# Performance work log

Hardware: AMD Instinct MI355X
Metric: run time of the kernel (lower is better)

The kernel has to match this reference:

```python
import jax, jax.numpy as jnp
import numpy as np

N = 50000
E = 800000
IN_DIM = 128
HID = 128
HEADS = 8
OUT_DIM = 64
NEG_SLOPE = 0.2


def setup_inputs() -> dict:
    key = jax.random.key(0)
    ks = jax.random.split(key, 10)
    x = jax.random.normal(ks[0], (N, IN_DIM), dtype=jnp.float32)
    edge_index = jax.random.randint(ks[1], (2, E), 0, N, dtype=jnp.int64)
    c1 = HID // HEADS  # 16 per-head channels, layer 1
    # layer 1 params (GATConv: lin has no bias; att_src/att_dst are [1,H,C])
    W1 = jax.random.normal(ks[2], (IN_DIM, HEADS * c1), dtype=jnp.float32) * 0.1
    att_src1 = jax.random.normal(ks[3], (1, HEADS, c1), dtype=jnp.float32) * 0.1
    att_dst1 = jax.random.normal(ks[4], (1, HEADS, c1), dtype=jnp.float32) * 0.1
    b1 = jnp.zeros((HEADS * c1,), dtype=jnp.float32)  # concat=True -> bias size H*C
    # layer 2 params (heads=1, concat=False)
    W2 = jax.random.normal(ks[5], (HID, OUT_DIM), dtype=jnp.float32) * 0.1
    att_src2 = jax.random.normal(ks[6], (1, 1, OUT_DIM), dtype=jnp.float32) * 0.1
    att_dst2 = jax.random.normal(ks[7], (1, 1, OUT_DIM), dtype=jnp.float32) * 0.1
    b2 = jnp.zeros((OUT_DIM,), dtype=jnp.float32)
    return {"x": x, "edge_index": edge_index,
            "W1": W1, "att_src1": att_src1, "att_dst1": att_dst1, "b1": b1,
            "W2": W2, "att_src2": att_src2, "att_dst2": att_dst2, "b2": b2}


def _gat_conv(x, src, dst, W, att_src, att_dst, bias, heads, concat):
    n = x.shape[0]
    c = W.shape[1] // heads
    h = (x @ W).reshape(n, heads, c)                      # [N,H,C]
    a_src = jnp.sum(h * att_src, axis=-1)                 # [N,H]
    a_dst = jnp.sum(h * att_dst, axis=-1)                 # [N,H]
    e = a_src[src] + a_dst[dst]                           # [E,H]
    e = jnp.where(e > 0, e, NEG_SLOPE * e)                # leaky_relu
    # segment softmax over incoming edges of each dst node
    m = jax.ops.segment_max(e, dst, num_segments=n)       # [N,H]
    ex = jnp.exp(e - m[dst])
    denom = jax.ops.segment_sum(ex, dst, num_segments=n)  # [N,H]
    alpha = ex / (denom[dst] + 1e-16)                     # [E,H]
    msg = h[src] * alpha[:, :, None]                      # [E,H,C]
    out = jax.ops.segment_sum(msg, dst, num_segments=n)   # [N,H,C]
    out = out.reshape(n, heads * c) if concat else out.mean(axis=1)
    return out + bias


def reference(x, edge_index, W1, att_src1, att_dst1, b1, W2, att_src2, att_dst2, b2):
    # add self-loops (PyG GATConv default add_self_loops=True)
    loops = jnp.arange(N, dtype=edge_index.dtype)
    src = jnp.concatenate([edge_index[0], loops])
    dst = jnp.concatenate([edge_index[1], loops])
    h = _gat_conv(x, src, dst, W1, att_src1, att_dst1, b1, HEADS, True)
    h = jax.nn.elu(h)
    out = _gat_conv(h, src, dst, W2, att_src2, att_dst2, b2, 1, False)
    return jax.nn.log_softmax(out, axis=1)
```

## Files before the change

### kernel.cpp

```cpp
#include <hip/hip_runtime.h>
#include <math.h>

#define N_NODES 50000
#define E_EDGES 800000
#define ET      (E_EDGES + N_NODES)
#define IN_DIM  128
#define HID     128
#define HEADS   8
#define C1      16
#define OUT_DIM 64
#define NEG_SLOPE 0.2f
#define LOG2E   1.4426950408889634f

#define TILE    8192
#define NT      ((ET + TILE - 1) / TILE)
#define NB      ((N_NODES + 255) / 256)

#define CONV_BLOCKS (N_NODES * IN_DIM / 4 / 256)
#define PREP_BLOCKS 112
#define MEGA_A (NT + CONV_BLOCKS + PREP_BLOCKS)
#define L1T_BLOCKS ((N_NODES + 63) / 64)
#define MEGA_B (NB + L1T_BLOCKS)
#define FUSE_BLOCKS ((N_NODES + 15) / 16)

typedef unsigned int uint32;
typedef __attribute__((ext_vector_type(8))) short bf16x8;
typedef __attribute__((ext_vector_type(4))) float f32x4;
typedef __attribute__((ext_vector_type(2))) float f32x2;

static __device__ __forceinline__ unsigned short f2bf(float f) {
    uint32 u = __float_as_uint(f);
    u += 0x7FFFu + ((u >> 16) & 1u);
    return (unsigned short)(u >> 16);
}

static __device__ __forceinline__ unsigned char f2fp8(float f) {
    int pk = __builtin_amdgcn_cvt_pk_fp8_f32(f, f, 0, false);
    return (unsigned char)(pk & 0xFF);
}


__global__ __launch_bounds__(256) void prep_all(
        const int* __restrict__ dst, int* __restrict__ cnt,
        const float* __restrict__ x, unsigned short* __restrict__ xb,
        const float* __restrict__ W1, const float* __restrict__ as1,
        const float* __restrict__ ad1, const float* __restrict__ W2,
        const float* __restrict__ as2, const float* __restrict__ ad2,
        unsigned short* __restrict__ w1t, unsigned short* __restrict__ p1t,
        unsigned short* __restrict__ w2t, unsigned short* __restrict__ p2t) {
    __shared__ int hist[NB];
    int blk = blockIdx.x, t = threadIdx.x;
    if (blk < NT) {
        for (int b = t; b < NB; b += 256) hist[b] = 0;
        __syncthreads();
        int base = blk * TILE;
        #pragma unroll
        for (int it = 0; it < TILE / 256; ++it) {
            int i = base + it * 256 + t;
            if (i < ET) {
                int d = (i < E_EDGES) ? dst[i] : (i - E_EDGES);
                atomicAdd(&hist[d >> 8], 1);
            }
        }
        __syncthreads();
        for (int b = t; b < NB; b += 256) cnt[blk * NB + b] = hist[b];
    } else if (blk < NT + CONV_BLOCKS) {
        int i = (blk - NT) * 256 + t;
        float4 v = ((const float4*)x)[i];
        ushort4 o;
        o.x = f2bf(v.x); o.y = f2bf(v.y); o.z = f2bf(v.z); o.w = f2bf(v.w);
        ((ushort4*)xb)[i] = o;
    } else {
        int b = blk - NT - CONV_BLOCKS;
        if (b < 64) {
            int i = b * 256 + t;
            int n = i >> 7, k = i & 127;
            w1t[n * IN_DIM + k] = f2bf(W1[k * HID + n]);
        } else if (b < 96) {
            int i = (b - 64) * 256 + t;
            int n = i >> 7, k = i & 127;
            w2t[n * HID + k] = f2bf(W2[k * OUT_DIM + n]);
        } else if (b < 104) {
            int i = (b - 96) * 256 + t;
            int j = i >> 7, k = i & 127;
            int hh = j & 7;
            const float* a = (j < 8) ? as1 : ad1;
            float acc = 0.f;
            #pragma unroll
            for (int c = 0; c < C1; ++c)
                acc = fmaf(W1[k * HID + hh * C1 + c], a[hh * C1 + c], acc);
            p1t[j * IN_DIM + k] = f2bf(acc * LOG2E);
        } else {
            int i = (b - 104) * 256 + t;
            int j = i >> 7, k = i & 127;
            if (j < 2) {
                const float* a = (j == 0) ? as2 : ad2;
                float acc = 0.f;
                #pragma unroll
                for (int c = 0; c < OUT_DIM; ++c)
                    acc = fmaf(W2[k * OUT_DIM + c], a[c], acc);
                p2t[j * HID + k] = f2bf(acc * LOG2E);
            } else {
                p2t[j * HID + k] = 0;
            }
        }
    }
}


__global__ __launch_bounds__(256) void bucket_scatter(
        const int* __restrict__ src, const int* __restrict__ dst,
        const int* __restrict__ cnt, int* __restrict__ bucketStart,
        uint32* __restrict__ pairs) {
    __shared__ int lcur[NB];
    __shared__ int sscan[256];
    int t = threadIdx.x;
    int tile = blockIdx.x;

    int run = 0, total = 0;
    if (t < NB) {
        for (int k = 0; k < NT; ++k) {
            int c = cnt[k * NB + t];
            if (k < tile) run += c;
            total += c;
        }
    }
    sscan[t] = (t < NB) ? total : 0;
    __syncthreads();
    #pragma unroll
    for (int off = 1; off < 256; off <<= 1) {
        int add = (t >= off) ? sscan[t - off] : 0;
        __syncthreads();
        sscan[t] += add;
        __syncthreads();
    }
    int bstart = sscan[t] - total;
    if (t < NB) {
        lcur[t] = bstart + run;
        if (tile == 0) bucketStart[t] = bstart;
    }
    if (tile == 0 && t == 0) bucketStart[NB] = ET;
    __syncthreads();

    int base = tile * TILE;
    #pragma unroll
    for (int it = 0; it < TILE / 256; ++it) {
        int i = base + it * 256 + t;
        if (i < ET) {
            int s, d;
            if (i < E_EDGES) { s = src[i]; d = dst[i]; }
            else             { s = d = i - E_EDGES; }
            int pos = atomicAdd(&lcur[d >> 8], 1);
            pairs[pos] = ((uint32)s << 8) | (uint32)(d & 255);
        }
    }
}


__global__ __launch_bounds__(256) void build_l1t(
        const uint32* __restrict__ pairs, const int* __restrict__ bucketStart,
        int* __restrict__ row_start, int* __restrict__ csr_src,
        const unsigned short* __restrict__ xb, const unsigned short* __restrict__ w1t,
        const unsigned short* __restrict__ p1t, unsigned char* __restrict__ h1f,
        float* __restrict__ a_src, float* __restrict__ a_dst) {
    __shared__ int sdeg[256];
    __shared__ int sscan[256];
    int t = threadIdx.x;
    if (blockIdx.x < NB) {
        int b = blockIdx.x;
        int beg = bucketStart[b], end = bucketStart[b + 1];
        sdeg[t] = 0;
        __syncthreads();
        for (int j = beg + t; j < end; j += 256)
            atomicAdd(&sdeg[pairs[j] & 255u], 1);
        __syncthreads();
        int v = sdeg[t];
        sscan[t] = v;
        __syncthreads();
        #pragma unroll
        for (int off = 1; off < 256; off <<= 1) {
            int add = (t >= off) ? sscan[t - off] : 0;
            __syncthreads();
            sscan[t] += add;
            __syncthreads();
        }
        int pos0 = beg + sscan[t] - v;
        int n = b * 256 + t;
        if (n < N_NODES) row_start[n] = pos0;
        if (b == 0 && t == 0) row_start[N_NODES] = ET;
        __syncthreads();
        sscan[t] = pos0;
        __syncthreads();
        for (int j = beg + t; j < end; j += 256) {
            uint32 p = pairs[j];
            int pos = atomicAdd(&sscan[p & 255u], 1);
            csr_src[pos] = (int)(p >> 8);
        }
        return;
    }
    int bb = blockIdx.x - NB;
    int w = t >> 6, lane = t & 63;
    int l15 = lane & 15, quad = lane >> 4;
    int n0 = bb * 64 + w * 16;
    int mrow = n0 + l15;
    int mload = (mrow < N_NODES) ? mrow : (N_NODES - 1);

    bf16x8 af[4];
    #pragma unroll
    for (int s = 0; s < 4; ++s)
        af[s] = *(const bf16x8*)&xb[(size_t)mload * IN_DIM + s * 32 + quad * 8];

    #pragma unroll
    for (int tt = 0; tt < 9; ++tt) {
        const unsigned short* Brow = (tt < 8) ? &w1t[(tt * 16 + l15) * IN_DIM]
                                              : &p1t[l15 * IN_DIM];
        f32x4 acc = {0.f, 0.f, 0.f, 0.f};
        #pragma unroll
        for (int s = 0; s < 4; ++s) {
            bf16x8 bf = *(const bf16x8*)&Brow[s * 32 + quad * 8];
            acc = __builtin_amdgcn_mfma_f32_16x16x32_bf16(af[s], bf, acc, 0, 0, 0);
        }
        int nodeb = n0 + quad * 4;
        if (tt < 8) {
            int ch = tt * 16 + l15;
            #pragma unroll
            for (int r = 0; r < 4; ++r)
                if (nodeb + r < N_NODES)
                    h1f[(size_t)(nodeb + r) * HID + ch] = f2fp8(acc[r]);
        } else {
            #pragma unroll
            for (int r = 0; r < 4; ++r) {
                if (nodeb + r < N_NODES) {
                    if (l15 < 8) a_src[(nodeb + r) * HEADS + l15] = acc[r];
                    else         a_dst[(nodeb + r) * HEADS + (l15 - 8)] = acc[r];
                }
            }
        }
    }
}


__global__ __launch_bounds__(256) void l1agg_l2t(
        const unsigned char* __restrict__ h1f, const float* __restrict__ a_src,
        const float* __restrict__ a_dst, const int* __restrict__ row_start,
        const int* __restrict__ csr_src, const float* __restrict__ b1,
        const unsigned short* __restrict__ w2t, const unsigned short* __restrict__ p2t,
        unsigned char* __restrict__ h2f, float* __restrict__ a_src2,
        float* __restrict__ a_dst2) {
    __shared__ unsigned short ha[16][128];
    __shared__ int sdeg16[16];
    __shared__ unsigned char perm[16];
    int t = threadIdx.x;
    int w = t >> 6;
    uint32 lane = t & 63;
    uint32 quarter = lane >> 4;
    uint32 lane16 = lane & 15;
    int n0blk = blockIdx.x * 16;

    if (t < 16) {
        int n = n0blk + t;
        int nc = (n < N_NODES) ? n : (N_NODES - 1);
        sdeg16[t] = row_start[nc + 1] - row_start[nc];
    }
    __syncthreads();
    if (t < 16) {
        int d = sdeg16[t];
        int r = 0;
        #pragma unroll
        for (int j = 0; j < 16; ++j) {
            int dj = sdeg16[j];
            r += (dj < d) || (dj == d && j < t);
        }
        perm[r] = (unsigned char)t;
    }
    __syncthreads();

    {
        uint32 c0 = lane16 * 8u;
        uint32 h = lane16 >> 1;
        int n_local = (int)perm[w * 4 + (int)quarter];
        int n = n0blk + n_local;
        int nc = (n < N_NODES) ? n : (N_NODES - 1);
        int beg = row_start[nc], end = row_start[nc + 1];
        int cnt = end - beg;
        int kmax = cnt;
        kmax = max(kmax, __shfl_xor(kmax, 16, 64));
        kmax = max(kmax, __shfl_xor(kmax, 32, 64));
        float adst = a_dst[nc * HEADS + h];
        float l = 0.f;
        float a0 = 0.f, a1 = 0.f, a2 = 0.f, a3 = 0.f;
        float a4 = 0.f, a5 = 0.f, a6 = 0.f, a7 = 0.f;

        auto edge = [&](float e0, uint2 u0, bool live) {
            float e = e0 + adst;
            e = fmaxf(e, NEG_SLOPE * e);
            e = live ? e : -10000.f;
            float p = exp2f(e);
            l += p;
            f32x2 f01 = __builtin_amdgcn_cvt_pk_f32_fp8((int)u0.x, false);
            f32x2 f23 = __builtin_amdgcn_cvt_pk_f32_fp8((int)u0.x, true);
            f32x2 f45 = __builtin_amdgcn_cvt_pk_f32_fp8((int)u0.y, false);
            f32x2 f67 = __builtin_amdgcn_cvt_pk_f32_fp8((int)u0.y, true);
            a0 = fmaf(p, f01[0], a0);
            a1 = fmaf(p, f01[1], a1);
            a2 = fmaf(p, f23[0], a2);
            a3 = fmaf(p, f23[1], a3);
            a4 = fmaf(p, f45[0], a4);
            a5 = fmaf(p, f45[1], a5);
            a6 = fmaf(p, f67[0], a6);
            a7 = fmaf(p, f67[1], a7);
        };

        int k = 0;
        for (; k + 8 <= kmax; k += 8) {
            uint32 ss[8]; float ee[8]; uint2 uu[8];
            #pragma unroll
            for (int q = 0; q < 8; ++q) {
                int j = beg + k + q;
                int jc = (j < end) ? j : (end - 1);
                ss[q] = (uint32)csr_src[jc];
            }
            #pragma unroll
            for (int q = 0; q < 8; ++q) ee[q] = a_src[ss[q] * 8u + h];
            #pragma unroll
            for (int q = 0; q < 8; ++q) uu[q] = *(const uint2*)&h1f[(ss[q] << 7) + c0];
            #pragma unroll
            for (int q = 0; q < 8; ++q) edge(ee[q], uu[q], k + q < cnt);
        }
        for (; k < kmax; k += 4) {
            uint32 ss[4]; float ee[4]; uint2 uu[4];
            #pragma unroll
            for (int q = 0; q < 4; ++q) {
                int j = beg + k + q;
                int jc = (j < end) ? j : (end - 1);
                ss[q] = (uint32)csr_src[jc];
            }
            #pragma unroll
            for (int q = 0; q < 4; ++q) ee[q] = a_src[ss[q] * 8u + h];
            #pragma unroll
            for (int q = 0; q < 4; ++q) uu[q] = *(const uint2*)&h1f[(ss[q] << 7) + c0];
            #pragma unroll
            for (int q = 0; q < 4; ++q) edge(ee[q], uu[q], k + q < cnt);
        }

        float inv = 1.f / (l + 1e-16f);
        float v0 = a0 * inv + b1[c0 + 0];
        float v1 = a1 * inv + b1[c0 + 1];
        float v2 = a2 * inv + b1[c0 + 2];
        float v3 = a3 * inv + b1[c0 + 3];
        float v4 = a4 * inv + b1[c0 + 4];
        float v5 = a5 * inv + b1[c0 + 5];
        float v6 = a6 * inv + b1[c0 + 6];
        float v7 = a7 * inv + b1[c0 + 7];
        v0 = v0 > 0.f ? v0 : (__expf(v0) - 1.f);
        v1 = v1 > 0.f ? v1 : (__expf(v1) - 1.f);
        v2 = v2 > 0.f ? v2 : (__expf(v2) - 1.f);
        v3 = v3 > 0.f ? v3 : (__expf(v3) - 1.f);
        v4 = v4 > 0.f ? v4 : (__expf(v4) - 1.f);
        v5 = v5 > 0.f ? v5 : (__expf(v5) - 1.f);
        v6 = v6 > 0.f ? v6 : (__expf(v6) - 1.f);
        v7 = v7 > 0.f ? v7 : (__expf(v7) - 1.f);
        uint4 packed;
        packed.x = (uint32)f2bf(v0) | ((uint32)f2bf(v1) << 16);
        packed.y = (uint32)f2bf(v2) | ((uint32)f2bf(v3) << 16);
        packed.z = (uint32)f2bf(v4) | ((uint32)f2bf(v5) << 16);
        packed.w = (uint32)f2bf(v6) | ((uint32)f2bf(v7) << 16);
        uint32 g = lane16 ^ ((uint32)n_local & 15u);
        *(uint4*)&ha[n_local][g * 8] = packed;
    }
    __syncthreads();

    {
        int l15 = (int)lane16, quad = (int)quarter;
        int n0 = n0blk;
        int nloc = l15;

        bf16x8 af[4];
        #pragma unroll
        for (int s = 0; s < 4; ++s) {
            uint32 g = (uint32)(s * 4 + quad) ^ (uint32)l15;
            af[s] = *(const bf16x8*)&ha[nloc][g * 8];
        }

        #pragma unroll
        for (int pass = 0; pass < 2; ++pass) {
            if (pass == 1 && w != 0) break;
            int tt = (pass == 0) ? w : 4;
            const unsigned short* Brow = (tt < 4) ? &w2t[(tt * 16 + l15) * HID]
                                                  : &p2t[l15 * HID];
            f32x4 acc = {0.f, 0.f, 0.f, 0.f};
            #pragma unroll
            for (int s = 0; s < 4; ++s) {
                bf16x8 bf = *(const bf16x8*)&Brow[s * 32 + quad * 8];
                acc = __builtin_amdgcn_mfma_f32_16x16x32_bf16(af[s], bf, acc, 0, 0, 0);
            }
            int nodeb = n0 + quad * 4;
            if (tt < 4) {
                int ch = tt * 16 + l15;
                #pragma unroll
                for (int r = 0; r < 4; ++r)
                    if (nodeb + r < N_NODES)
                        h2f[(size_t)(nodeb + r) * OUT_DIM + ch] = f2fp8(acc[r]);
            } else {
                #pragma unroll
                for (int r = 0; r < 4; ++r) {
                    if (nodeb + r < N_NODES) {
                        if (l15 == 0) a_src2[nodeb + r] = acc[r];
                        else if (l15 == 1) a_dst2[nodeb + r] = acc[r];
                    }
                }
            }
        }
    }
}


__global__ __launch_bounds__(128) void l2_aggregate(
        const unsigned char* __restrict__ h2f, const float* __restrict__ a_src2,
        const float* __restrict__ a_dst2, const int* __restrict__ row_start,
        const int* __restrict__ csr_src, const float* __restrict__ b2,
        float* __restrict__ out) {
    __shared__ int sdeg8[8];
    __shared__ int perm8[8];
    int t = threadIdx.x;
    int w = t >> 6;
    uint32 lane = t & 63;
    uint32 quarter = lane >> 4;
    uint32 lane16 = lane & 15;
    int nbase = blockIdx.x * 8;
    if (t < 8)
        sdeg8[t] = row_start[nbase + t + 1] - row_start[nbase + t];
    __syncthreads();
    if (t < 8) {
        int d = sdeg8[t];
        int r = 0;
        #pragma unroll
        for (int j = 0; j < 8; ++j) {
            int dj = sdeg8[j];
            r += (dj < d) || (dj == d && j < t);
        }
        perm8[r] = t;
    }
    __syncthreads();
    int n = nbase + perm8[w * 4 + (int)quarter];
    uint32 c0 = lane16 * 4u;
    int beg = row_start[n], end = row_start[n + 1];
    int cnt = end - beg;
    int kmax = cnt;
    kmax = max(kmax, __shfl_xor(kmax, 16, 64));
    kmax = max(kmax, __shfl_xor(kmax, 32, 64));
    float adst = a_dst2[n];
    float l = 0.f, a0 = 0.f, a1 = 0.f, a2 = 0.f, a3 = 0.f;

    for (int k = 0; k < kmax; k += 4) {
        uint32 ss[4]; float ee[4]; uint32 uu[4];
        #pragma unroll
        for (int q = 0; q < 4; ++q) {
            int j = beg + k + q;
            int jc = (j < end) ? j : (end - 1);
            ss[q] = (uint32)csr_src[jc];
        }
        #pragma unroll
        for (int q = 0; q < 4; ++q) ee[q] = a_src2[ss[q]];
        #pragma unroll
        for (int q = 0; q < 4; ++q) uu[q] = *(const uint32*)&h2f[(ss[q] << 6) + c0];
        #pragma unroll
        for (int q = 0; q < 4; ++q) {
            float e = ee[q] + adst;
            e = fmaxf(e, NEG_SLOPE * e);
            e = (k + q < cnt) ? e : -10000.f;
            float p = exp2f(e);
            l += p;
            f32x2 f01 = __builtin_amdgcn_cvt_pk_f32_fp8((int)uu[q], false);
            f32x2 f23 = __builtin_amdgcn_cvt_pk_f32_fp8((int)uu[q], true);
            a0 = fmaf(p, f01[0], a0);
            a1 = fmaf(p, f01[1], a1);
            a2 = fmaf(p, f23[0], a2);
            a3 = fmaf(p, f23[1], a3);
        }
    }

    float inv = 1.f / (l + 1e-16f);
    float o0 = a0 * inv + b2[c0 + 0];
    float o1 = a1 * inv + b2[c0 + 1];
    float o2 = a2 * inv + b2[c0 + 2];
    float o3 = a3 * inv + b2[c0 + 3];
    float mx = fmaxf(fmaxf(o0, o1), fmaxf(o2, o3));
    #pragma unroll
    for (int m = 8; m > 0; m >>= 1) mx = fmaxf(mx, __shfl_xor(mx, m, 16));
    float ex = __expf(o0 - mx) + __expf(o1 - mx) + __expf(o2 - mx) + __expf(o3 - mx);
    #pragma unroll
    for (int m = 8; m > 0; m >>= 1) ex += __shfl_xor(ex, m, 16);
    float lse = mx + __logf(ex);
    float4 o = make_float4(o0 - lse, o1 - lse, o2 - lse, o3 - lse);
    *(float4*)&out[(size_t)n * OUT_DIM + c0] = o;
}


extern "C" void kernel_launch(void* const* d_in, const int* in_sizes, int n_in,
                              void* d_out, int out_size, void* d_ws, size_t ws_size,
                              hipStream_t stream) {
    const float* x   = (const float*)d_in[0];
    const int*   ei  = (const int*)d_in[1];
    const float* W1  = (const float*)d_in[2];
    const float* as1 = (const float*)d_in[3];
    const float* ad1 = (const float*)d_in[4];
    const float* b1  = (const float*)d_in[5];
    const float* W2  = (const float*)d_in[6];
    const float* as2 = (const float*)d_in[7];
    const float* ad2 = (const float*)d_in[8];
    const float* b2  = (const float*)d_in[9];
    float* out = (float*)d_out;

    const int* src = ei;
    const int* dst = ei + E_EDGES;

    char* ws = (char*)d_ws;
    size_t off = 0;
    auto alloc = [&](size_t bytes) -> void* {
        void* p = ws + off;
        off += (bytes + 255) & ~size_t(255);
        return p;
    };
    unsigned short* xb     = (unsigned short*)alloc((size_t)N_NODES * IN_DIM * 2);
    unsigned char*  h1f    = (unsigned char*)alloc((size_t)N_NODES * HID);
    unsigned char*  h2f    = (unsigned char*)alloc((size_t)N_NODES * OUT_DIM);
    unsigned short* w1t    = (unsigned short*)alloc((size_t)HID * IN_DIM * 2);
    unsigned short* p1t    = (unsigned short*)alloc((size_t)16 * IN_DIM * 2);
    unsigned short* w2t    = (unsigned short*)alloc((size_t)OUT_DIM * HID * 2);
    unsigned short* p2t    = (unsigned short*)alloc((size_t)16 * HID * 2);
    float* a_src1    = (float*)alloc((size_t)N_NODES * HEADS * 4);
    float* a_dst1    = (float*)alloc((size_t)N_NODES * HEADS * 4);
    float* a_src2    = (float*)alloc((size_t)N_NODES * 4);
    float* a_dst2    = (float*)alloc((size_t)N_NODES * 4);
    int*   row_start = (int*)alloc((size_t)(N_NODES + 1) * 4);
    int*   csr_src   = (int*)alloc((size_t)ET * 4);
    uint32* pairs    = (uint32*)alloc((size_t)ET * 4);
    int*   cnt       = (int*)alloc((size_t)NB * NT * 4);
    int*   bucketStart = (int*)alloc((size_t)(NB + 1) * 4);

    prep_all<<<MEGA_A, 256, 0, stream>>>(dst, cnt, x, xb, W1, as1, ad1,
                                         W2, as2, ad2, w1t, p1t, w2t, p2t);
    bucket_scatter<<<NT, 256, 0, stream>>>(src, dst, cnt, bucketStart, pairs);
    build_l1t<<<MEGA_B, 256, 0, stream>>>(pairs, bucketStart, row_start, csr_src,
                                          xb, w1t, p1t, h1f, a_src1, a_dst1);
    l1agg_l2t<<<FUSE_BLOCKS, 256, 0, stream>>>(h1f, a_src1, a_dst1, row_start, csr_src,
                                               b1, w2t, p2t, h2f, a_src2, a_dst2);
    l2_aggregate<<<N_NODES / 8, 128, 0, stream>>>(h2f, a_src2, a_dst2, row_start, csr_src, b2, out);
}
```

Before: 191.9 us.

## Split layer-1 transform across scatter and bucket kernels; prefetch CSR indices

Moves the layer-1 MFMA transform into a shared device function and splits its blocks between the bucket-scatter kernel (391 blocks) and the CSR build kernel (the rest). This balances work across the two launches so the transform overlaps the lightweight scatter phase. Both aggregation kernels now prefetch the next batch of 8 CSR source indices while the current batch is processed. The layer-2 aggregation also moves to 256-thread blocks of 16 nodes with an 8-edge unrolled loop. The changes add register pressure, and the gains depend on scheduling across kernels.

Result: faster. 187.8 us (-2.1%).

```diff
diff --git a/kernel.cpp b/kernel.cpp
--- a/kernel.cpp
+++ b/kernel.cpp
@@ -20,7 +20,8 @@
 #define PREP_BLOCKS 112
 #define MEGA_A (NT + CONV_BLOCKS + PREP_BLOCKS)
 #define L1T_BLOCKS ((N_NODES + 63) / 64)
-#define MEGA_B (NB + L1T_BLOCKS)
+#define L1TA 391
+#define L1TB (L1T_BLOCKS - L1TA)
 #define FUSE_BLOCKS ((N_NODES + 15) / 16)
 
 typedef unsigned int uint32;
@@ -108,13 +109,66 @@
 }
 
 
-__global__ __launch_bounds__(256) void bucket_scatter(
+static __device__ __forceinline__ void l1_transform_body(
+        int bb, int t,
+        const unsigned short* __restrict__ xb, const unsigned short* __restrict__ w1t,
+        const unsigned short* __restrict__ p1t, unsigned char* __restrict__ h1f,
+        float* __restrict__ a_src, float* __restrict__ a_dst) {
+    int w = t >> 6, lane = t & 63;
+    int l15 = lane & 15, quad = lane >> 4;
+    int n0 = bb * 64 + w * 16;
+    int mrow = n0 + l15;
+    int mload = (mrow < N_NODES) ? mrow : (N_NODES - 1);
+
+    bf16x8 af[4];
+    #pragma unroll
+    for (int s = 0; s < 4; ++s)
+        af[s] = *(const bf16x8*)&xb[(size_t)mload * IN_DIM + s * 32 + quad * 8];
+
+    #pragma unroll
+    for (int tt = 0; tt < 9; ++tt) {
+        const unsigned short* Brow = (tt < 8) ? &w1t[(tt * 16 + l15) * IN_DIM]
+                                              : &p1t[l15 * IN_DIM];
+        f32x4 acc = {0.f, 0.f, 0.f, 0.f};
+        #pragma unroll
+        for (int s = 0; s < 4; ++s) {
+            bf16x8 bf = *(const bf16x8*)&Brow[s * 32 + quad * 8];
+            acc = __builtin_amdgcn_mfma_f32_16x16x32_bf16(af[s], bf, acc, 0, 0, 0);
+        }
+        int nodeb = n0 + quad * 4;
+        if (tt < 8) {
+            int ch = tt * 16 + l15;
+            #pragma unroll
+            for (int r = 0; r < 4; ++r)
+                if (nodeb + r < N_NODES)
+                    h1f[(size_t)(nodeb + r) * HID + ch] = f2fp8(acc[r]);
+        } else {
+            #pragma unroll
+            for (int r = 0; r < 4; ++r) {
+                if (nodeb + r < N_NODES) {
+                    if (l15 < 8) a_src[(nodeb + r) * HEADS + l15] = acc[r];
+                    else         a_dst[(nodeb + r) * HEADS + (l15 - 8)] = acc[r];
+                }
+            }
+        }
+    }
+}
+
+
+__global__ __launch_bounds__(256) void scatter_l1ta(
         const int* __restrict__ src, const int* __restrict__ dst,
         const int* __restrict__ cnt, int* __restrict__ bucketStart,
-        uint32* __restrict__ pairs) {
+        uint32* __restrict__ pairs,
+        const unsigned short* __restrict__ xb, const unsigned short* __restrict__ w1t,
+        const unsigned short* __restrict__ p1t, unsigned char* __restrict__ h1f,
+        float* __restrict__ a_src, float* __restrict__ a_dst) {
     __shared__ int lcur[NB];
     __shared__ int sscan[256];
     int t = threadIdx.x;
+    if (blockIdx.x >= NT) {
+        l1_transform_body(blockIdx.x - NT, t, xb, w1t, p1t, h1f, a_src, a_dst);
+        return;
+    }
     int tile = blockIdx.x;
 
     int run = 0, total = 0;
@@ -157,7 +211,7 @@
 }
 
 
-__global__ __launch_bounds__(256) void build_l1t(
+__global__ __launch_bounds__(256) void bucket_l1tb(
         const uint32* __restrict__ pairs, const int* __restrict__ bucketStart,
         int* __restrict__ row_start, int* __restrict__ csr_src,
         const unsigned short* __restrict__ xb, const unsigned short* __restrict__ w1t,
@@ -166,76 +220,38 @@
     __shared__ int sdeg[256];
     __shared__ int sscan[256];
     int t = threadIdx.x;
-    if (blockIdx.x < NB) {
-        int b = blockIdx.x;
-        int beg = bucketStart[b], end = bucketStart[b + 1];
-        sdeg[t] = 0;
+    if (blockIdx.x >= NB) {
+        l1_transform_body(blockIdx.x - NB + L1TA, t, xb, w1t, p1t, h1f, a_src, a_dst);
+        return;
+    }
+    int b = blockIdx.x;
+    int beg = bucketStart[b], end = bucketStart[b + 1];
+    sdeg[t] = 0;
+    __syncthreads();
+    for (int j = beg + t; j < end; j += 256)
+        atomicAdd(&sdeg[pairs[j] & 255u], 1);
+    __syncthreads();
+    int v = sdeg[t];
+    sscan[t] = v;
+    __syncthreads();
+    #pragma unroll
+    for (int off = 1; off < 256; off <<= 1) {
+        int add = (t >= off) ? sscan[t - off] : 0;
         __syncthreads();
-        for (int j = beg + t; j < end; j += 256)
-            atomicAdd(&sdeg[pairs[j] & 255u], 1);
+        sscan[t] += add;
         __syncthreads();
-        int v = sdeg[t];
-        sscan[t] = v;
-        __syncthreads();
-        #pragma unroll
-        for (int off = 1; off < 256; off <<= 1) {
-            int add = (t >= off) ? sscan[t - off] : 0;
-            __syncthreads();
-            sscan[t] += add;
-            __syncthreads();
-        }
-        int pos0 = beg + sscan[t] - v;
-        int n = b * 256 + t;
-        if (n < N_NODES) row_start[n] = pos0;
-        if (b == 0 && t == 0) row_start[N_NODES] = ET;
-        __syncthreads();
-        sscan[t] = pos0;
-        __syncthreads();
-        for (int j = beg + t; j < end; j += 256) {
-            uint32 p = pairs[j];
-            int pos = atomicAdd(&sscan[p & 255u], 1);
-            csr_src[pos] = (int)(p >> 8);
-        }
-        return;
-    }
-    int bb = blockIdx.x - NB;
-    int w = t >> 6, lane = t & 63;
-    int l15 = lane & 15, quad = lane >> 4;
-    int n0 = bb * 64 + w * 16;
-    int mrow = n0 + l15;
-    int mload = (mrow < N_NODES) ? mrow : (N_NODES - 1);
-
-    bf16x8 af[4];
-    #pragma unroll
-    for (int s = 0; s < 4; ++s)
-        af[s] = *(const bf16x8*)&xb[(size_t)mload * IN_DIM + s * 32 + quad * 8];
-
-    #pragma unroll
-    for (int tt = 0; tt < 9; ++tt) {
-        const unsigned short* Brow = (tt < 8) ? &w1t[(tt * 16 + l15) * IN_DIM]
-                                              : &p1t[l15 * IN_DIM];
-        f32x4 acc = {0.f, 0.f, 0.f, 0.f};
-        #pragma unroll
-        for (int s = 0; s < 4; ++s) {
-            bf16x8 bf = *(const bf16x8*)&Brow[s * 32 + quad * 8];
-            acc = __builtin_amdgcn_mfma_f32_16x16x32_bf16(af[s], bf, acc, 0, 0, 0);
-        }
-        int nodeb = n0 + quad * 4;
-        if (tt < 8) {
-            int ch = tt * 16 + l15;
-            #pragma unroll
-            for (int r = 0; r < 4; ++r)
-                if (nodeb + r < N_NODES)
-                    h1f[(size_t)(nodeb + r) * HID + ch] = f2fp8(acc[r]);
-        } else {
-            #pragma unroll
-            for (int r = 0; r < 4; ++r) {
-                if (nodeb + r < N_NODES) {
-                    if (l15 < 8) a_src[(nodeb + r) * HEADS + l15] = acc[r];
-                    else         a_dst[(nodeb + r) * HEADS + (l15 - 8)] = acc[r];
-                }
-            }
-        }
+    }
+    int pos0 = beg + sscan[t] - v;
+    int n = b * 256 + t;
+    if (n < N_NODES) row_start[n] = pos0;
+    if (b == 0 && t == 0) row_start[N_NODES] = ET;
+    __syncthreads();
+    sscan[t] = pos0;
+    __syncthreads();
+    for (int j = beg + t; j < end; j += 256) {
+        uint32 p = pairs[j];
+        int pos = atomicAdd(&sscan[p & 255u], 1);
+        csr_src[pos] = (int)(p >> 8);
     }
 }
 
@@ -312,18 +328,32 @@
         };
 
         int k = 0;
+        uint32 ssn[8];
+        if (k + 8 <= kmax) {
+            #pragma unroll
+            for (int q = 0; q < 8; ++q) {
+                int j = beg + q;
+                int jc = (j < end) ? j : (end - 1);
+                ssn[q] = (uint32)csr_src[jc];
+            }
+        }
         for (; k + 8 <= kmax; k += 8) {
             uint32 ss[8]; float ee[8]; uint2 uu[8];
             #pragma unroll
-            for (int q = 0; q < 8; ++q) {
-                int j = beg + k + q;
-                int jc = (j < end) ? j : (end - 1);
-                ss[q] = (uint32)csr_src[jc];
-            }
+            for (int q = 0; q < 8; ++q) ss[q] = ssn[q];
             #pragma unroll
             for (int q = 0; q < 8; ++q) ee[q] = a_src[ss[q] * 8u + h];
             #pragma unroll
             for (int q = 0; q < 8; ++q) uu[q] = *(const uint2*)&h1f[(ss[q] << 7) + c0];
+            int kn = k + 8;
+            if (kn + 8 <= kmax) {
+                #pragma unroll
+                for (int q = 0; q < 8; ++q) {
+                    int j = beg + kn + q;
+                    int jc = (j < end) ? j : (end - 1);
+                    ssn[q] = (uint32)csr_src[jc];
+                }
+            }
             #pragma unroll
             for (int q = 0; q < 8; ++q) edge(ee[q], uu[q], k + q < cnt);
         }
@@ -415,34 +445,34 @@
 }
 
 
-__global__ __launch_bounds__(128) void l2_aggregate(
+__global__ __launch_bounds__(256) void l2_aggregate(
         const unsigned char* __restrict__ h2f, const float* __restrict__ a_src2,
         const float* __restrict__ a_dst2, const int* __restrict__ row_start,
         const int* __restrict__ csr_src, const float* __restrict__ b2,
         float* __restrict__ out) {
-    __shared__ int sdeg8[8];
-    __shared__ int perm8[8];
+    __shared__ int sdeg16[16];
+    __shared__ int perm16[16];
     int t = threadIdx.x;
     int w = t >> 6;
     uint32 lane = t & 63;
     uint32 quarter = lane >> 4;
     uint32 lane16 = lane & 15;
-    int nbase = blockIdx.x * 8;
-    if (t < 8)
-        sdeg8[t] = row_start[nbase + t + 1] - row_start[nbase + t];
-    __syncthreads();
-    if (t < 8) {
-        int d = sdeg8[t];
+    int nbase = blockIdx.x * 16;
+    if (t < 16)
+        sdeg16[t] = row_start[nbase + t + 1] - row_start[nbase + t];
+    __syncthreads();
+    if (t < 16) {
+        int d = sdeg16[t];
         int r = 0;
         #pragma unroll
-        for (int j = 0; j < 8; ++j) {
-            int dj = sdeg8[j];
+        for (int j = 0; j < 16; ++j) {
+            int dj = sdeg16[j];
             r += (dj < d) || (dj == d && j < t);
         }
-        perm8[r] = t;
-    }
-    __syncthreads();
-    int n = nbase + perm8[w * 4 + (int)quarter];
+        perm16[r] = t;
+    }
+    __syncthreads();
+    int n = nbase + perm16[w * 4 + (int)quarter];
     uint32 c0 = lane16 * 4u;
     int beg = row_start[n], end = row_start[n + 1];
     int cnt = end - beg;
@@ -452,7 +482,51 @@
     float adst = a_dst2[n];
     float l = 0.f, a0 = 0.f, a1 = 0.f, a2 = 0.f, a3 = 0.f;
 
-    for (int k = 0; k < kmax; k += 4) {
+    auto edge2 = [&](float e0, uint32 u0, bool live) {
+        float e = e0 + adst;
+        e = fmaxf(e, NEG_SLOPE * e);
+        e = live ? e : -10000.f;
+        float p = exp2f(e);
+        l += p;
+        f32x2 f01 = __builtin_amdgcn_cvt_pk_f32_fp8((int)u0, false);
+        f32x2 f23 = __builtin_amdgcn_cvt_pk_f32_fp8((int)u0, true);
+        a0 = fmaf(p, f01[0], a0);
+        a1 = fmaf(p, f01[1], a1);
+        a2 = fmaf(p, f23[0], a2);
+        a3 = fmaf(p, f23[1], a3);
+    };
+
+    int k = 0;
+    uint32 ssn[8];
+    if (k + 8 <= kmax) {
+        #pragma unroll
+        for (int q = 0; q < 8; ++q) {
+            int j = beg + q;
+            int jc = (j < end) ? j : (end - 1);
+            ssn[q] = (uint32)csr_src[jc];
+        }
+    }
+    for (; k + 8 <= kmax; k += 8) {
+        uint32 ss[8]; float ee[8]; uint32 uu[8];
+        #pragma unroll
+        for (int q = 0; q < 8; ++q) ss[q] = ssn[q];
+        #pragma unroll
+        for (int q = 0; q < 8; ++q) ee[q] = a_src2[ss[q]];
+        #pragma unroll
+        for (int q = 0; q < 8; ++q) uu[q] = *(const uint32*)&h2f[(ss[q] << 6) + c0];
+        int kn = k + 8;
+        if (kn + 8 <= kmax) {
+            #pragma unroll
+            for (int q = 0; q < 8; ++q) {
+                int j = beg + kn + q;
+                int jc = (j < end) ? j : (end - 1);
+                ssn[q] = (uint32)csr_src[jc];
+            }
+        }
+        #pragma unroll
+        for (int q = 0; q < 8; ++q) edge2(ee[q], uu[q], k + q < cnt);
+    }
+    for (; k < kmax; k += 4) {
         uint32 ss[4]; float ee[4]; uint32 uu[4];
         #pragma unroll
         for (int q = 0; q < 4; ++q) {
@@ -465,19 +539,7 @@
         #pragma unroll
         for (int q = 0; q < 4; ++q) uu[q] = *(const uint32*)&h2f[(ss[q] << 6) + c0];
         #pragma unroll
-        for (int q = 0; q < 4; ++q) {
-            float e = ee[q] + adst;
-            e = fmaxf(e, NEG_SLOPE * e);
-            e = (k + q < cnt) ? e : -10000.f;
-            float p = exp2f(e);
-            l += p;
-            f32x2 f01 = __builtin_amdgcn_cvt_pk_f32_fp8((int)uu[q], false);
-            f32x2 f23 = __builtin_amdgcn_cvt_pk_f32_fp8((int)uu[q], true);
-            a0 = fmaf(p, f01[0], a0);
-            a1 = fmaf(p, f01[1], a1);
-            a2 = fmaf(p, f23[0], a2);
-            a3 = fmaf(p, f23[1], a3);
-        }
+        for (int q = 0; q < 4; ++q) edge2(ee[q], uu[q], k + q < cnt);
     }
 
     float inv = 1.f / (l + 1e-16f);
@@ -541,10 +603,12 @@
 
     prep_all<<<MEGA_A, 256, 0, stream>>>(dst, cnt, x, xb, W1, as1, ad1,
                                          W2, as2, ad2, w1t, p1t, w2t, p2t);
-    bucket_scatter<<<NT, 256, 0, stream>>>(src, dst, cnt, bucketStart, pairs);
-    build_l1t<<<MEGA_B, 256, 0, stream>>>(pairs, bucketStart, row_start, csr_src,
-                                          xb, w1t, p1t, h1f, a_src1, a_dst1);
+    scatter_l1ta<<<NT + L1TA, 256, 0, stream>>>(src, dst, cnt, bucketStart, pairs,
+                                                xb, w1t, p1t, h1f, a_src1, a_dst1);
+    bucket_l1tb<<<NB + L1TB, 256, 0, stream>>>(pairs, bucketStart, row_start, csr_src,
+                                               xb, w1t, p1t, h1f, a_src1, a_dst1);
     l1agg_l2t<<<FUSE_BLOCKS, 256, 0, stream>>>(h1f, a_src1, a_dst1, row_start, csr_src,
                                                b1, w2t, p2t, h2f, a_src2, a_dst2);
-    l2_aggregate<<<N_NODES / 8, 128, 0, stream>>>(h2f, a_src2, a_dst2, row_start, csr_src, b2, out);
-}
+    l2_aggregate<<<FUSE_BLOCKS, 256, 0, stream>>>(h2f, a_src2, a_dst2, row_start,
+                                                  csr_src, b2, out);
+}
```
